# Optimization experiments

Hardware: AMD Instinct MI355X
Metric: run time of the kernel (lower is better)

## Reference

```python
import jax, jax.numpy as jnp
import numpy as np

B, L, HID = 8, 1025, 1024
H, KV, DH = 16, 4, 64
EPS = 1e-6
ROPE_BASE = 10000.0


def _rms_norm(x, w):
    var = jnp.mean(jnp.square(x), axis=-1, keepdims=True)
    return x * jax.lax.rsqrt(var + EPS) * w


def _rotate_half(x):
    x1, x2 = jnp.split(x, 2, axis=-1)
    return jnp.concatenate([-x2, x1], axis=-1)


def _rope_cache(seq_len, dim):
    inv_freq = 1.0 / (ROPE_BASE ** (jnp.arange(0, dim, 2, dtype=jnp.float32) / dim))
    pos = jnp.arange(seq_len, dtype=jnp.float32)
    freqs = pos[:, None] * inv_freq[None, :]            # [L_img, dim/2]
    emb = jnp.concatenate([freqs, freqs], axis=-1)       # [L_img, dim]
    return jnp.cos(emb), jnp.sin(emb)


def setup_inputs() -> dict:
    key = jax.random.key(0)
    ks = jax.random.split(key, 5)
    s_in = 1.0
    s_q = float(np.sqrt(2.0 / (HID + H * DH)))
    s_kv = float(np.sqrt(2.0 / (HID + KV * DH)))
    s_o = float(np.sqrt(2.0 / (H * DH + HID)) / np.sqrt(2.0))
    return {
        "inputs": jax.random.normal(ks[0], (B, L, HID), jnp.float32) * s_in,
        "Wq": jax.random.normal(ks[1], (H * DH, HID), jnp.float32) * s_q,
        "Wk": jax.random.normal(ks[2], (KV * DH, HID), jnp.float32) * s_kv,
        "Wv": jax.random.normal(ks[3], (KV * DH, HID), jnp.float32) * s_kv,
        "Wo": jax.random.normal(ks[4], (HID, H * DH), jnp.float32) * s_o,
        "q_norm_w": jnp.ones((DH,), jnp.float32),
        "k_norm_w": jnp.ones((DH,), jnp.float32),
    }


def reference(inputs, Wq, Wk, Wv, Wo, q_norm_w, k_norm_w):
    b, l, _ = inputs.shape
    # projections (torch Linear: x @ W.T), reshape to heads, QK RMSNorm
    q = (inputs @ Wq.T).reshape(b, l, H, DH)
    k = (inputs @ Wk.T).reshape(b, l, KV, DH)
    v = (inputs @ Wv.T).reshape(b, l, KV, DH)
    q = _rms_norm(q, q_norm_w).transpose(0, 2, 1, 3)    # [B,H,L,DH]
    k = _rms_norm(k, k_norm_w).transpose(0, 2, 1, 3)    # [B,KV,L,DH]
    v = v.transpose(0, 2, 1, 3)                          # [B,KV,L,DH]

    # RoPE only on image tokens (skip first action token)
    l_img = l - 1
    cos, sin = _rope_cache(l_img, DH)                    # [L_img, DH]
    cos = cos[None, None].astype(q.dtype)
    sin = sin[None, None].astype(q.dtype)
    q_img = q[:, :, 1:]
    k_img = k[:, :, 1:]
    q = jnp.concatenate([q[:, :, :1], q_img * cos + _rotate_half(q_img) * sin], axis=2)
    k = jnp.concatenate([k[:, :, :1], k_img * cos + _rotate_half(k_img) * sin], axis=2)

    # GQA: repeat kv heads
    rep = H // KV
    k = jnp.repeat(k, rep, axis=1)                       # [B,H,L,DH]
    v = jnp.repeat(v, rep, axis=1)

    # manual attention: NOTE no 1/sqrt(DH) scaling (faithful to source)
    scores = jnp.einsum("bhqd,bhkd->bhqk", q, k)
    attn = jax.nn.softmax(scores.astype(jnp.float32), axis=-1).astype(q.dtype)
    out = jnp.einsum("bhqk,bhkd->bhqd", attn, v)         # [B,H,L,DH]
    out = out.transpose(0, 2, 1, 3).reshape(b, l, H * DH)
    return out @ Wo.T
```

## Files before the change

### kernel.cpp

```cpp
#include <hip/hip_runtime.h>
#include <hip/hip_bf16.h>

using bf16 = __hip_bfloat16;
typedef __bf16 bf16x8 __attribute__((ext_vector_type(8)));
typedef float f32x4 __attribute__((ext_vector_type(4)));
typedef short short8 __attribute__((ext_vector_type(8)));
typedef unsigned short ushort4v __attribute__((ext_vector_type(4)));

#define MFMA16(a, b, c) __builtin_amdgcn_mfma_f32_16x16x32_bf16((a), (b), (c), 0, 0, 0)

constexpr int B_ = 8, L_ = 1025, H_ = 16, KV_ = 4;
constexpr int LKP_ = 1088;
constexpr int M_ = B_ * L_;

constexpr int NX = 8396800, NWQ = 1048576, NWK = 262144, NWV = 262144,
              NWO = 1048576, NNW = 64;

__device__ __forceinline__ void gl_lds16(const bf16* g, bf16* l) {
  __builtin_amdgcn_global_load_lds(
      (const __attribute__((address_space(1))) void*)g,
      (__attribute__((address_space(3))) void*)l, 16, 0, 0);
}

__global__ __launch_bounds__(64) void detect_dtype(const unsigned short* qw_raw,
                                                   int* flag) {
  if (threadIdx.x == 0) flag[0] = (qw_raw[0] == 0x3F80) ? 0 : 1;
}

__global__ __launch_bounds__(256) void convert_all(
    const void* s0, const void* s1, const void* s2, const void* s3,
    const void* s4, const void* s5, const void* s6,
    bf16* d0, bf16* d1, bf16* d2, bf16* d3, bf16* d4, bf16* d5, bf16* d6,
    const int* flag) {
  const int f = *flag;
  const int tid = blockIdx.x * blockDim.x + threadIdx.x;
  const int stride = gridDim.x * blockDim.x;
  auto conv = [&](const void* s, bf16* d, int n) {
    if (f) {
      const float* sf = (const float*)s;
      for (int i = tid; i < n; i += stride) d[i] = __float2bfloat16(sf[i]);
    } else {
      const unsigned short* su = (const unsigned short*)s;
      unsigned short* du = (unsigned short*)d;
      for (int i = tid; i < n; i += stride) du[i] = su[i];
    }
  };
  conv(s0, d0, NX);
  conv(s1, d1, NWQ);
  conv(s2, d2, NWK);
  conv(s3, d3, NWV);
  conv(s4, d4, NWO);
  conv(s5, d5, NNW);
  conv(s6, d6, NNW);
}

__global__ __launch_bounds__(256) void zero_pads(bf16* Kb, bf16* VT) {
  const int idx = blockIdx.x * 256 + threadIdx.x;
  const bf16 z = __float2bfloat16(0.f);
  {
    const int g = idx / 4032, rem = idx % 4032;
    const int r = rem >> 6, d = rem & 63;
    Kb[((size_t)g * LKP_ + 1025 + r) * 64 + d] = z;
  }
  {
    const int row = idx / 63, c = idx % 63;
    VT[(size_t)row * LKP_ + 1025 + c] = z;
  }
}

template <int EPI>
__global__ __launch_bounds__(256) void gemm_bt(
    const bf16* __restrict__ X, const bf16* __restrict__ W0,
    const bf16* __restrict__ W1, const bf16* __restrict__ W2,
    void* __restrict__ O0, bf16* __restrict__ O1, bf16* __restrict__ O2,
    const bf16* __restrict__ qw, const bf16* __restrict__ kw,
    const int* flag) {
  const int m0 = blockIdx.x * 128;
  const int n0 = blockIdx.y * 128;

  int outf32 = 0;
  if constexpr (EPI == 0) outf32 = *flag;

  const bf16* W;
  int nw0;
  if constexpr (EPI == 0) {
    W = W0; nw0 = n0;
  } else {
    if (n0 < 1024)      { W = W0; nw0 = n0; }
    else if (n0 < 1280) { W = W1; nw0 = n0 - 1024; }
    else                { W = W2; nw0 = n0 - 1280; }
  }

  __shared__ bf16 As[128 * 32];
  __shared__ bf16 Bs[128 * 32];

  const int tid = threadIdx.x;
  const int lane = tid & 63, wid = tid >> 6;
  const int wr = wid >> 1, wc = wid & 1;
  const int lo = lane & 15, g = lane >> 4;

  const f32x4 zero4 = {0.f, 0.f, 0.f, 0.f};
  f32x4 acc[4][4];
#pragma unroll
  for (int i = 0; i < 4; ++i)
#pragma unroll
    for (int j = 0; j < 4; ++j) acc[i][j] = zero4;

  const int srow = tid >> 2, scol8 = (tid & 3) * 8;
  int xr0 = m0 + srow;      if (xr0 > M_ - 1) xr0 = M_ - 1;
  int xr1 = m0 + 64 + srow; if (xr1 > M_ - 1) xr1 = M_ - 1;
  const bf16* xp0 = X + (size_t)xr0 * 1024 + scol8;
  const bf16* xp1 = X + (size_t)xr1 * 1024 + scol8;
  const bf16* wp0 = W + (size_t)(nw0 + srow) * 1024 + scol8;
  const bf16* wp1 = W + (size_t)(nw0 + 64 + srow) * 1024 + scol8;

  for (int kt = 0; kt < 32; ++kt) {
    gl_lds16(xp0, &As[(size_t)tid * 8]);
    gl_lds16(xp1, &As[2048 + (size_t)tid * 8]);
    gl_lds16(wp0, &Bs[(size_t)tid * 8]);
    gl_lds16(wp1, &Bs[2048 + (size_t)tid * 8]);
    xp0 += 32; xp1 += 32; wp0 += 32; wp1 += 32;
    __syncthreads();

    bf16x8 a[4], bb[4];
#pragma unroll
    for (int i = 0; i < 4; ++i)
      a[i] = *reinterpret_cast<const bf16x8*>(&As[(wr * 64 + i * 16 + lo) * 32 + g * 8]);
#pragma unroll
    for (int j = 0; j < 4; ++j)
      bb[j] = *reinterpret_cast<const bf16x8*>(&Bs[(wc * 64 + j * 16 + lo) * 32 + g * 8]);
#pragma unroll
    for (int i = 0; i < 4; ++i)
#pragma unroll
      for (int j = 0; j < 4; ++j)
        acc[i][j] = MFMA16(a[i], bb[j], acc[i][j]);
    __syncthreads();
  }

  const bool qkreg = (EPI == 1) && (n0 < 1280);
  float wv[4];
  float invf0 = 0.f, invf1 = 0.f;
  if (qkreg) {
    const bf16* w = (n0 < 1024) ? qw : kw;
#pragma unroll
    for (int j = 0; j < 4; ++j) wv[j] = __bfloat162float(w[j * 16 + lo]);
    constexpr float c = -0.41524101186092029f;
    invf0 = exp2f((float)lo * c);
    invf1 = invf0 * exp2f(16.f * c);
  }

#pragma unroll
  for (int i = 0; i < 4; ++i) {
#pragma unroll
    for (int ii = 0; ii < 4; ++ii) {
      const int m = m0 + wr * 64 + i * 16 + g * 4 + ii;
      if (m >= M_) continue;
      const int b = m / L_;
      const int l = m % L_;
      float fv[4];
#pragma unroll
      for (int j = 0; j < 4; ++j) fv[j] = acc[i][j][ii];

      if (qkreg) {
#pragma unroll
        for (int j = 0; j < 4; ++j)
          fv[j] = __bfloat162float(__float2bfloat16(fv[j]));
        float ss = fv[0] * fv[0] + fv[1] * fv[1] + fv[2] * fv[2] + fv[3] * fv[3];
        ss += __shfl_xor(ss, 1);
        ss += __shfl_xor(ss, 2);
        ss += __shfl_xor(ss, 4);
        ss += __shfl_xor(ss, 8);
        const float r = rsqrtf(ss * (1.f / 64.f) + 1e-6f);
#pragma unroll
        for (int j = 0; j < 4; ++j) fv[j] *= r * wv[j];
        if (l > 0) {
          const float pos = (float)(l - 1);
          float sn0, cs0, sn1, cs1;
          __sincosf(pos * invf0, &sn0, &cs0);
          __sincosf(pos * invf1, &sn1, &cs1);
          const float a0 = fv[0], a2 = fv[2];
          fv[0] = a0 * cs0 - a2 * sn0;
          fv[2] = a2 * cs0 + a0 * sn0;
          const float a1 = fv[1], a3 = fv[3];
          fv[1] = a1 * cs1 - a3 * sn1;
          fv[3] = a3 * cs1 + a1 * sn1;
        }
      }

#pragma unroll
      for (int j = 0; j < 4; ++j) {
        const int n = n0 + wc * 64 + j * 16 + lo;
        const float f = fv[j];
        if constexpr (EPI == 0) {
          if (outf32) ((float*)O0)[(size_t)m * 1024 + n] = f;
          else        ((bf16*)O0)[(size_t)m * 1024 + n] = __float2bfloat16(f);
        } else {
          const bf16 v = __float2bfloat16(f);
          if (n < 1024) {
            ((bf16*)O0)[((size_t)(b * H_ + (n >> 6)) * L_ + l) * 64 + (n & 63)] = v;
          } else if (n < 1280) {
            const int c2 = n - 1024;
            O1[((size_t)(b * KV_ + (c2 >> 6)) * LKP_ + l) * 64 + (c2 & 63)] = v;
          } else {
            const int c2 = n - 1280;
            O2[((size_t)(b * KV_ + (c2 >> 6)) * 64 + (c2 & 63)) * LKP_ + l] = v;
          }
        }
      }
    }
  }
}

__global__ __launch_bounds__(512) void attn(
    const bf16* __restrict__ Q, const bf16* __restrict__ Kt,
    const bf16* __restrict__ VT, bf16* __restrict__ AO) {
  const int tid = threadIdx.x, lane = tid & 63, w = tid >> 6;
  const int lo = lane & 15, g = lane >> 4;
  const int qt = blockIdx.x, h = blockIdx.y, b = blockIdx.z;
  const int kv = h >> 2;

  __shared__ unsigned short Ks[64][72];
  __shared__ unsigned short Vs[64][72];
  __shared__ unsigned short Ps[8][16][72];

  const bf16* qbase = Q + (size_t)(b * H_ + h) * L_ * 64;
  int qrow = qt * 128 + w * 16 + lo;
  if (qrow > L_ - 1) qrow = L_ - 1;
  const bf16x8 qf0 = *reinterpret_cast<const bf16x8*>(qbase + (size_t)qrow * 64 + g * 8);
  const bf16x8 qf1 = *reinterpret_cast<const bf16x8*>(qbase + (size_t)qrow * 64 + 32 + g * 8);

  const f32x4 zero4 = {0.f, 0.f, 0.f, 0.f};
  f32x4 o[4];
  float mi = -3e38f, li = 0.f;
#pragma unroll
  for (int i = 0; i < 4; ++i) o[i] = zero4;

  const int sr = tid >> 3;
  const int scol = (tid & 7) * 8;
  const bf16* kbase = Kt + ((size_t)(b * KV_ + kv) * LKP_ + sr) * 64 + scol;
  const bf16* vbase = VT + ((size_t)(b * KV_ + kv) * 64 + sr) * LKP_ + scol;

  for (int kt = 0; kt < 17; ++kt) {
    const int k0 = kt * 64;
    const short8 ka = *reinterpret_cast<const short8*>(kbase + (size_t)k0 * 64);
    const short8 va = *reinterpret_cast<const short8*>(vbase + k0);
    __syncthreads();
    *reinterpret_cast<short8*>(&Ks[sr][scol]) = ka;
    *reinterpret_cast<short8*>(&Vs[sr][scol]) = va;
    __syncthreads();

    f32x4 s[4];
#pragma unroll
    for (int kb = 0; kb < 4; ++kb) {
      f32x4 t = zero4;
      const bf16x8 ka0 = *reinterpret_cast<const bf16x8*>(&Ks[kb * 16 + lo][g * 8]);
      const bf16x8 ka1 = *reinterpret_cast<const bf16x8*>(&Ks[kb * 16 + lo][32 + g * 8]);
      t = MFMA16(ka0, qf0, t);
      t = MFMA16(ka1, qf1, t);
      s[kb] = t;
    }
    if (kt == 16) {
#pragma unroll
      for (int kb = 0; kb < 4; ++kb)
#pragma unroll
        for (int i = 0; i < 4; ++i)
          if (k0 + kb * 16 + g * 4 + i >= L_) s[kb][i] = -1e30f;
    }

    float t0 = fmaxf(fmaxf(s[0][0], s[0][1]), fmaxf(s[0][2], s[0][3]));
    float t1 = fmaxf(fmaxf(s[1][0], s[1][1]), fmaxf(s[1][2], s[1][3]));
    float t2 = fmaxf(fmaxf(s[2][0], s[2][1]), fmaxf(s[2][2], s[2][3]));
    float t3 = fmaxf(fmaxf(s[3][0], s[3][1]), fmaxf(s[3][2], s[3][3]));
    float tm = fmaxf(fmaxf(t0, t1), fmaxf(t2, t3));
    tm = fmaxf(tm, __shfl_xor(tm, 16));
    tm = fmaxf(tm, __shfl_xor(tm, 32));
    const float mn = fmaxf(mi, tm);
    const float sc = __expf(mi - mn);
    mi = mn;
#pragma unroll
    for (int kb = 0; kb < 4; ++kb)
#pragma unroll
      for (int i = 0; i < 4; ++i) s[kb][i] = __expf(s[kb][i] - mn);
    float p0 = (s[0][0] + s[0][1]) + (s[0][2] + s[0][3]);
    float p1 = (s[1][0] + s[1][1]) + (s[1][2] + s[1][3]);
    float p2 = (s[2][0] + s[2][1]) + (s[2][2] + s[2][3]);
    float p3 = (s[3][0] + s[3][1]) + (s[3][2] + s[3][3]);
    float ps = (p0 + p1) + (p2 + p3);
    ps += __shfl_xor(ps, 16);
    ps += __shfl_xor(ps, 32);
    li = li * sc + ps;
#pragma unroll
    for (int db = 0; db < 4; ++db)
#pragma unroll
      for (int i = 0; i < 4; ++i) o[db][i] *= sc;

#pragma unroll
    for (int kb = 0; kb < 4; ++kb) {
      ushort4v pk;
#pragma unroll
      for (int i = 0; i < 4; ++i)
        pk[i] = __builtin_bit_cast(unsigned short, __float2bfloat16(s[kb][i]));
      *reinterpret_cast<ushort4v*>(&Ps[w][lo][kb * 16 + 4 * g]) = pk;
    }

    const bf16x8 pb0 = *reinterpret_cast<const bf16x8*>(&Ps[w][lo][g * 8]);
    const bf16x8 pb1 = *reinterpret_cast<const bf16x8*>(&Ps[w][lo][32 + g * 8]);
#pragma unroll
    for (int db = 0; db < 4; ++db) {
      const bf16x8 va0 = *reinterpret_cast<const bf16x8*>(&Vs[db * 16 + lo][g * 8]);
      const bf16x8 va1 = *reinterpret_cast<const bf16x8*>(&Vs[db * 16 + lo][32 + g * 8]);
      o[db] = MFMA16(va0, pb0, o[db]);
      o[db] = MFMA16(va1, pb1, o[db]);
    }
  }

  const int qr = qt * 128 + w * 16 + lo;
  if (qr < L_) {
    const float inv = 1.f / li;
    unsigned* base = (unsigned*)(AO + ((size_t)b * L_ + qr) * 1024 + h * 64);
#pragma unroll
    for (int db = 0; db < 4; ++db) {
#pragma unroll
      for (int i2 = 0; i2 < 4; i2 += 2) {
        const unsigned u0 = __builtin_bit_cast(unsigned short,
                                __float2bfloat16(o[db][i2] * inv));
        const unsigned u1 = __builtin_bit_cast(unsigned short,
                                __float2bfloat16(o[db][i2 + 1] * inv));
        base[(db * 16 + 4 * g + i2) >> 1] = u0 | (u1 << 16);
      }
    }
  }
}

extern "C" void kernel_launch(void* const* d_in, const int* in_sizes, int n_in,
                              void* d_out, int out_size, void* d_ws, size_t ws_size,
                              hipStream_t stream) {
  (void)in_sizes; (void)n_in; (void)out_size; (void)ws_size;

  char* wsb = (char*)d_ws;
  int* flagp = (int*)wsb;
  bf16* cX  = (bf16*)(wsb + 16);
  bf16* cWq = cX + NX;
  bf16* cWk = cWq + NWQ;
  bf16* cWv = cWk + NWK;
  bf16* cWo = cWv + NWV;
  bf16* cqw = cWo + NWO;
  bf16* ckw = cqw + NNW;
  bf16* Qb  = ckw + NNW;
  bf16* Kb  = Qb  + (size_t)B_ * H_ * L_ * 64;
  bf16* VTb = Kb  + (size_t)B_ * KV_ * LKP_ * 64;
  bf16* AOb = VTb + (size_t)B_ * KV_ * 64 * LKP_;

  detect_dtype<<<1, 64, 0, stream>>>((const unsigned short*)d_in[5], flagp);
  convert_all<<<2048, 256, 0, stream>>>(
      d_in[0], d_in[1], d_in[2], d_in[3], d_in[4], d_in[5], d_in[6],
      cX, cWq, cWk, cWv, cWo, cqw, ckw, flagp);
  zero_pads<<<504, 256, 0, stream>>>(Kb, VTb);

  gemm_bt<1><<<dim3(65, 12), 256, 0, stream>>>(cX, cWq, cWk, cWv, Qb, Kb, VTb,
                                               cqw, ckw, nullptr);
  attn<<<dim3(9, 16, 8), 512, 0, stream>>>(Qb, Kb, VTb, AOb);
  gemm_bt<0><<<dim3(65, 8), 256, 0, stream>>>(AOb, cWo, nullptr, nullptr, d_out,
                                              nullptr, nullptr, nullptr, nullptr,
                                              flagp);
}
```

Baseline: 248.2 us.

## Vectorize conversion, swizzle LDS, widen GEMM K-tile, XCD remap, lazy softmax rescale

The conversion kernel now moves eight elements per thread iteration with vector loads and stores. The GEMM uses a 64-wide K tile with XOR-swizzled LDS layout and an XCD-aware 1D block remapping. The attention kernel replaces padded LDS arrays with XOR-swizzled layouts and skips the online-softmax rescale when no lane's max increases. Together these target LDS bank conflicts, L2 locality across XCDs, loop overhead and wasted ALU work, at the cost of more LDS per block and more complex indexing.

New measurement: 212.8 us. 1.17x faster.

```diff
diff --git a/kernel.cpp b/kernel.cpp
--- a/kernel.cpp
+++ b/kernel.cpp
@@ -20,6 +20,13 @@
   __builtin_amdgcn_global_load_lds(
       (const __attribute__((address_space(1))) void*)g,
       (__attribute__((address_space(3))) void*)l, 16, 0, 0);
+}
+
+template <int NWG>
+__device__ __forceinline__ int xcd_swz(int orig) {
+  constexpr int q = NWG >> 3, r = NWG & 7;
+  const int x = orig & 7, idx = orig >> 3;
+  return (x < r ? x * (q + 1) : r * (q + 1) + (x - r) * q) + idx;
 }
 
 __global__ __launch_bounds__(64) void detect_dtype(const unsigned short* qw_raw,
@@ -36,13 +43,24 @@
   const int tid = blockIdx.x * blockDim.x + threadIdx.x;
   const int stride = gridDim.x * blockDim.x;
   auto conv = [&](const void* s, bf16* d, int n) {
+    const int n8 = n >> 3;
     if (f) {
-      const float* sf = (const float*)s;
-      for (int i = tid; i < n; i += stride) d[i] = __float2bfloat16(sf[i]);
+      const f32x4* sf = (const f32x4*)s;
+      short8* dd = (short8*)d;
+      for (int i = tid; i < n8; i += stride) {
+        const f32x4 v0 = sf[2 * i], v1 = sf[2 * i + 1];
+        short8 o;
+#pragma unroll
+        for (int j = 0; j < 4; ++j) {
+          o[j]     = __builtin_bit_cast(short, __float2bfloat16(v0[j]));
+          o[j + 4] = __builtin_bit_cast(short, __float2bfloat16(v1[j]));
+        }
+        dd[i] = o;
+      }
     } else {
-      const unsigned short* su = (const unsigned short*)s;
-      unsigned short* du = (unsigned short*)d;
-      for (int i = tid; i < n; i += stride) du[i] = su[i];
+      const short8* su = (const short8*)s;
+      short8* dd = (short8*)d;
+      for (int i = tid; i < n8; i += stride) dd[i] = su[i];
     }
   };
   conv(s0, d0, NX);
@@ -68,15 +86,16 @@
   }
 }
 
-template <int EPI>
+template <int EPI, int NT, int NWG>
 __global__ __launch_bounds__(256) void gemm_bt(
     const bf16* __restrict__ X, const bf16* __restrict__ W0,
     const bf16* __restrict__ W1, const bf16* __restrict__ W2,
     void* __restrict__ O0, bf16* __restrict__ O1, bf16* __restrict__ O2,
     const bf16* __restrict__ qw, const bf16* __restrict__ kw,
     const int* flag) {
-  const int m0 = blockIdx.x * 128;
-  const int n0 = blockIdx.y * 128;
+  const int wg = xcd_swz<NWG>(blockIdx.x);
+  const int m0 = (wg / NT) * 128;
+  const int n0 = (wg % NT) * 128;
 
   int outf32 = 0;
   if constexpr (EPI == 0) outf32 = *flag;
@@ -91,8 +110,8 @@
     else                { W = W2; nw0 = n0 - 1280; }
   }
 
-  __shared__ bf16 As[128 * 32];
-  __shared__ bf16 Bs[128 * 32];
+  __shared__ bf16 As[128 * 64];
+  __shared__ bf16 Bs[128 * 64];
 
   const int tid = threadIdx.x;
   const int lane = tid & 63, wid = tid >> 6;
@@ -106,34 +125,45 @@
 #pragma unroll
     for (int j = 0; j < 4; ++j) acc[i][j] = zero4;
 
-  const int srow = tid >> 2, scol8 = (tid & 3) * 8;
-  int xr0 = m0 + srow;      if (xr0 > M_ - 1) xr0 = M_ - 1;
-  int xr1 = m0 + 64 + srow; if (xr1 > M_ - 1) xr1 = M_ - 1;
-  const bf16* xp0 = X + (size_t)xr0 * 1024 + scol8;
-  const bf16* xp1 = X + (size_t)xr1 * 1024 + scol8;
-  const bf16* wp0 = W + (size_t)(nw0 + srow) * 1024 + scol8;
-  const bf16* wp1 = W + (size_t)(nw0 + 64 + srow) * 1024 + scol8;
-
-  for (int kt = 0; kt < 32; ++kt) {
-    gl_lds16(xp0, &As[(size_t)tid * 8]);
-    gl_lds16(xp1, &As[2048 + (size_t)tid * 8]);
-    gl_lds16(wp0, &Bs[(size_t)tid * 8]);
-    gl_lds16(wp1, &Bs[2048 + (size_t)tid * 8]);
-    xp0 += 32; xp1 += 32; wp0 += 32; wp1 += 32;
+  const int rr = tid >> 3;
+  const int csw = ((tid & 7) ^ (rr & 7)) * 8;
+  const bf16* xp[4];
+  const bf16* wp[4];
+#pragma unroll
+  for (int is = 0; is < 4; ++is) {
+    int rx = m0 + rr + 32 * is;
+    if (rx > M_ - 1) rx = M_ - 1;
+    xp[is] = X + (size_t)rx * 1024 + csw;
+    wp[is] = W + (size_t)(nw0 + rr + 32 * is) * 1024 + csw;
+  }
+
+  for (int kt = 0; kt < 16; ++kt) {
+#pragma unroll
+    for (int is = 0; is < 4; ++is) {
+      gl_lds16(xp[is], &As[is * 2048 + (size_t)tid * 8]);
+      gl_lds16(wp[is], &Bs[is * 2048 + (size_t)tid * 8]);
+      xp[is] += 64; wp[is] += 64;
+    }
     __syncthreads();
 
-    bf16x8 a[4], bb[4];
-#pragma unroll
-    for (int i = 0; i < 4; ++i)
-      a[i] = *reinterpret_cast<const bf16x8*>(&As[(wr * 64 + i * 16 + lo) * 32 + g * 8]);
-#pragma unroll
-    for (int j = 0; j < 4; ++j)
-      bb[j] = *reinterpret_cast<const bf16x8*>(&Bs[(wc * 64 + j * 16 + lo) * 32 + g * 8]);
-#pragma unroll
-    for (int i = 0; i < 4; ++i)
+    bf16x8 a[2][4], bb[2][4];
+#pragma unroll
+    for (int kk = 0; kk < 2; ++kk) {
+      const int sw = ((4 * kk + g) ^ (lo & 7)) * 8;
+#pragma unroll
+      for (int i = 0; i < 4; ++i)
+        a[kk][i] = *reinterpret_cast<const bf16x8*>(&As[(wr * 64 + i * 16 + lo) * 64 + sw]);
 #pragma unroll
       for (int j = 0; j < 4; ++j)
-        acc[i][j] = MFMA16(a[i], bb[j], acc[i][j]);
+        bb[kk][j] = *reinterpret_cast<const bf16x8*>(&Bs[(wc * 64 + j * 16 + lo) * 64 + sw]);
+    }
+#pragma unroll
+    for (int kk = 0; kk < 2; ++kk)
+#pragma unroll
+      for (int i = 0; i < 4; ++i)
+#pragma unroll
+        for (int j = 0; j < 4; ++j)
+          acc[i][j] = MFMA16(a[kk][i], bb[kk][j], acc[i][j]);
     __syncthreads();
   }
 
@@ -219,9 +249,9 @@
   const int qt = blockIdx.x, h = blockIdx.y, b = blockIdx.z;
   const int kv = h >> 2;
 
-  __shared__ unsigned short Ks[64][72];
-  __shared__ unsigned short Vs[64][72];
-  __shared__ unsigned short Ps[8][16][72];
+  __shared__ unsigned short Ks[64 * 64];
+  __shared__ unsigned short Vs[64 * 64];
+  __shared__ unsigned short Ps[8 * 16 * 64];
 
   const bf16* qbase = Q + (size_t)(b * H_ + h) * L_ * 64;
   int qrow = qt * 128 + w * 16 + lo;
@@ -237,24 +267,29 @@
 
   const int sr = tid >> 3;
   const int scol = (tid & 7) * 8;
+  const int swcol = ((tid & 7) ^ (sr & 7)) * 8;
   const bf16* kbase = Kt + ((size_t)(b * KV_ + kv) * LKP_ + sr) * 64 + scol;
   const bf16* vbase = VT + ((size_t)(b * KV_ + kv) * 64 + sr) * LKP_ + scol;
+
+  const int sw0 = (g ^ (lo & 7)) * 8;
+  const int sw1 = ((4 | g) ^ (lo & 7)) * 8;
+  const int pswa = ((g >> 1) ^ (lo & 7));
 
   for (int kt = 0; kt < 17; ++kt) {
     const int k0 = kt * 64;
     const short8 ka = *reinterpret_cast<const short8*>(kbase + (size_t)k0 * 64);
     const short8 va = *reinterpret_cast<const short8*>(vbase + k0);
     __syncthreads();
-    *reinterpret_cast<short8*>(&Ks[sr][scol]) = ka;
-    *reinterpret_cast<short8*>(&Vs[sr][scol]) = va;
+    *reinterpret_cast<short8*>(&Ks[sr * 64 + swcol]) = ka;
+    *reinterpret_cast<short8*>(&Vs[sr * 64 + swcol]) = va;
     __syncthreads();
 
     f32x4 s[4];
 #pragma unroll
     for (int kb = 0; kb < 4; ++kb) {
       f32x4 t = zero4;
-      const bf16x8 ka0 = *reinterpret_cast<const bf16x8*>(&Ks[kb * 16 + lo][g * 8]);
-      const bf16x8 ka1 = *reinterpret_cast<const bf16x8*>(&Ks[kb * 16 + lo][32 + g * 8]);
+      const bf16x8 ka0 = *reinterpret_cast<const bf16x8*>(&Ks[(kb * 16 + lo) * 64 + sw0]);
+      const bf16x8 ka1 = *reinterpret_cast<const bf16x8*>(&Ks[(kb * 16 + lo) * 64 + sw1]);
       t = MFMA16(ka0, qf0, t);
       t = MFMA16(ka1, qf1, t);
       s[kb] = t;
@@ -274,13 +309,20 @@
     float tm = fmaxf(fmaxf(t0, t1), fmaxf(t2, t3));
     tm = fmaxf(tm, __shfl_xor(tm, 16));
     tm = fmaxf(tm, __shfl_xor(tm, 32));
-    const float mn = fmaxf(mi, tm);
-    const float sc = __expf(mi - mn);
-    mi = mn;
+    if (!__all(tm <= mi)) {
+      const float mn = fmaxf(mi, tm);
+      const float sc = __expf(mi - mn);
+      mi = mn;
+      li *= sc;
+#pragma unroll
+      for (int db = 0; db < 4; ++db)
+#pragma unroll
+        for (int i = 0; i < 4; ++i) o[db][i] *= sc;
+    }
 #pragma unroll
     for (int kb = 0; kb < 4; ++kb)
 #pragma unroll
-      for (int i = 0; i < 4; ++i) s[kb][i] = __expf(s[kb][i] - mn);
+      for (int i = 0; i < 4; ++i) s[kb][i] = __expf(s[kb][i] - mi);
     float p0 = (s[0][0] + s[0][1]) + (s[0][2] + s[0][3]);
     float p1 = (s[1][0] + s[1][1]) + (s[1][2] + s[1][3]);
     float p2 = (s[2][0] + s[2][1]) + (s[2][2] + s[2][3]);
@@ -288,11 +330,7 @@
     float ps = (p0 + p1) + (p2 + p3);
     ps += __shfl_xor(ps, 16);
     ps += __shfl_xor(ps, 32);
-    li = li * sc + ps;
-#pragma unroll
-    for (int db = 0; db < 4; ++db)
-#pragma unroll
-      for (int i = 0; i < 4; ++i) o[db][i] *= sc;
+    li += ps;
 
 #pragma unroll
     for (int kb = 0; kb < 4; ++kb) {
@@ -300,15 +338,18 @@
 #pragma unroll
       for (int i = 0; i < 4; ++i)
         pk[i] = __builtin_bit_cast(unsigned short, __float2bfloat16(s[kb][i]));
-      *reinterpret_cast<ushort4v*>(&Ps[w][lo][kb * 16 + 4 * g]) = pk;
-    }
-
-    const bf16x8 pb0 = *reinterpret_cast<const bf16x8*>(&Ps[w][lo][g * 8]);
-    const bf16x8 pb1 = *reinterpret_cast<const bf16x8*>(&Ps[w][lo][32 + g * 8]);
+      *reinterpret_cast<ushort4v*>(
+          &Ps[w * 1024 + lo * 64 + ((2 * kb) ^ pswa ^ (g >> 1) ^ (g >> 1)) * 8 +
+              (((2 * kb + (g >> 1)) ^ (lo & 7)) - ((2 * kb) ^ pswa ^ (g >> 1) ^ (g >> 1))) * 8 +
+              (g & 1) * 4]) = pk;
+    }
+
+    const bf16x8 pb0 = *reinterpret_cast<const bf16x8*>(&Ps[w * 1024 + lo * 64 + sw0]);
+    const bf16x8 pb1 = *reinterpret_cast<const bf16x8*>(&Ps[w * 1024 + lo * 64 + sw1]);
 #pragma unroll
     for (int db = 0; db < 4; ++db) {
-      const bf16x8 va0 = *reinterpret_cast<const bf16x8*>(&Vs[db * 16 + lo][g * 8]);
-      const bf16x8 va1 = *reinterpret_cast<const bf16x8*>(&Vs[db * 16 + lo][32 + g * 8]);
+      const bf16x8 va0 = *reinterpret_cast<const bf16x8*>(&Vs[(db * 16 + lo) * 64 + sw0]);
+      const bf16x8 va1 = *reinterpret_cast<const bf16x8*>(&Vs[(db * 16 + lo) * 64 + sw1]);
       o[db] = MFMA16(va0, pb0, o[db]);
       o[db] = MFMA16(va1, pb1, o[db]);
     }
@@ -357,10 +398,10 @@
       cX, cWq, cWk, cWv, cWo, cqw, ckw, flagp);
   zero_pads<<<504, 256, 0, stream>>>(Kb, VTb);
 
-  gemm_bt<1><<<dim3(65, 12), 256, 0, stream>>>(cX, cWq, cWk, cWv, Qb, Kb, VTb,
+  gemm_bt<1, 12, 780><<<780, 256, 0, stream>>>(cX, cWq, cWk, cWv, Qb, Kb, VTb,
                                                cqw, ckw, nullptr);
   attn<<<dim3(9, 16, 8), 512, 0, stream>>>(Qb, Kb, VTb, AOb);
-  gemm_bt<0><<<dim3(65, 8), 256, 0, stream>>>(AOb, cWo, nullptr, nullptr, d_out,
+  gemm_bt<0, 8, 520><<<520, 256, 0, stream>>>(AOb, cWo, nullptr, nullptr, d_out,
                                               nullptr, nullptr, nullptr, nullptr,
                                               flagp);
 }
```
